# Performance work log

Hardware: AMD Instinct MI355X
Metric: run time of the kernel (lower is better)

The kernel has to match this reference:

```python
import jax, jax.numpy as jnp
import numpy as np

N = 8192       # nodes == in_channels (diff matrix is NxN)
DF = 256       # feature dim of z
E = 65536      # edges (unused by forward, kept for signature fidelity)
M = 4096       # len(reliable_negatives)
NEG = 10       # neg_samples
STEPS = 10     # num_diffusion_steps
TEMP = 0.2


def setup_inputs() -> dict:
    key = jax.random.key(0)
    k1, k2, k3, k4, k5 = jax.random.split(key, 5)
    z = jax.random.normal(k1, (N, DF), dtype=jnp.float32)
    # learned parameter; init positive-uniform so row sums are well conditioned
    diff_matrix = jax.random.uniform(k2, (N, N), dtype=jnp.float32)
    edge_index = jax.random.randint(k3, (2, E), 0, N)
    reliable_negatives = jax.random.randint(k4, (M,), 0, N)
    # deterministic stand-in for torch.randint(0, len(reliable_negatives), (neg_samples,))
    neg_idx = jax.random.randint(k5, (NEG,), 0, M)
    return {"z": z, "diff_matrix": diff_matrix, "edge_index": edge_index,
            "reliable_negatives": reliable_negatives, "neg_idx": neg_idx}


def _l2norm(x):
    # F.normalize(dim=1): divide by L2 norm clamped at 1e-12
    n = jnp.sqrt(jnp.sum(x * x, axis=1, keepdims=True))
    return x / jnp.maximum(n, 1e-12)


def reference(z, diff_matrix, edge_index, reliable_negatives, neg_idx):
    # 10-step loop: mm(inverse(diag(rowsum)), M) == row-wise reciprocal scaling
    dm = diff_matrix
    for _ in range(STEPS):
        dm = dm / jnp.sum(dm, axis=1, keepdims=True)  # [N, N]
    # (normalized_diff_matrix with +eps*I is computed in the original but unused)

    anchor = z                       # [N, DF]
    positive = dm @ z                # [N, DF] diffused features
    negative = z[neg_idx]            # [NEG, DF]

    a = _l2norm(anchor)
    p = _l2norm(positive)
    n = _l2norm(negative)

    pos_sim = jnp.sum(a * p, axis=1) / TEMP                 # [N]
    neg_sim = jnp.exp(jnp.einsum('nd,kd->nk', a, n) / TEMP)  # [N, NEG]
    loss = -jnp.log(jnp.exp(pos_sim) / (jnp.exp(pos_sim) + neg_sim.sum(axis=1))).mean()
    return loss
```

## Files before the change

### kernel.cpp

```cpp
#include <hip/hip_runtime.h>
#include <hip/hip_bf16.h>


typedef float f32x4 __attribute__((ext_vector_type(4)));
typedef short s16x8 __attribute__((ext_vector_type(8)));

#define NN 8192
#define DFF 256
#define NNEG 10

__device__ __forceinline__ unsigned short f2bf(float x) {
  return __builtin_bit_cast(unsigned short, __float2bfloat16(x));
}

__device__ __forceinline__ float bf2f(unsigned short u) {
  return __builtin_bit_cast(float, (unsigned int)u << 16);
}

__device__ __forceinline__ void gload_lds16(const void* g, void* l) {
  __builtin_amdgcn_global_load_lds(
      (const __attribute__((address_space(1))) void*)(void*)g,
      (__attribute__((address_space(3))) void*)l, 16, 0, 0);
}

__device__ __forceinline__ float dot4(float4 a, float4 b) {
  return a.x * b.x + a.y * b.y + a.z * b.z + a.w * b.w;
}

__global__ void k_pack(const float* __restrict__ z,
                       unsigned short* __restrict__ zp) {
  __shared__ float tile[64][65];
  const int bx = blockIdx.x;
  const int by = blockIdx.y;
  const int t = threadIdx.x;
  const int lc = t & 63, lq = t >> 6;
#pragma unroll
  for (int p = 0; p < 16; ++p) {
    const int kr = lq * 16 + p;
    tile[kr][lc] = z[(size_t)(bx * 64 + kr) * DFF + by * 64 + lc];
  }
  __syncthreads();
#pragma unroll
  for (int p2 = 0; p2 < 2; ++p2) {
    const int ko = lq * 2 + p2;
    s16x8 v;
#pragma unroll
    for (int ke = 0; ke < 8; ++ke) v[ke] = (short)f2bf(tile[ko * 8 + ke][lc]);
    const int chunk = bx * 2 + (ko >> 2);
    const int kw = ko & 3;
    const int d = by * 64 + lc;
    *(s16x8*)(zp + (size_t)chunk * 8192 + kw * 2048 + d * 8) = v;
  }
}

__global__ __launch_bounds__(512, 2) void k_gemm(const float* __restrict__ dm,
                                                 const unsigned short* __restrict__ zp,
                                                 unsigned short* __restrict__ part,
                                                 int KS) {
  __shared__ __align__(16) unsigned short sA[2][4096];
  __shared__ __align__(16) unsigned short sB[2][8192];
  const int bx = blockIdx.x;
  const int mtile = bx & 63;
  const int ks = bx >> 6;
  const int klen = NN / KS;
  const int k0 = ks * klen;
  const int c0 = k0 >> 5;
  const int steps = klen / 32;
  const int tid = threadIdx.x;
  const int w = tid >> 6;
  const int l = tid & 63;
  const int m0 = mtile * 128;

  const int arow = w * 16 + (l & 15);
  const int akw = l >> 4;
  const float* asrc = dm + (size_t)(m0 + arow) * NN + k0 + akw * 8;

  const int r16 = l & 15, kw = l >> 4;
  const int wm = w >> 2, wn = w & 3;

  f32x4 acc[4][4] = {};
  float4 a0, a1;

#define LOAD_A(t_)                                                             \
  {                                                                            \
    a0 = *(const float4*)(asrc + (t_)*32);                                     \
    a1 = *(const float4*)(asrc + (t_)*32 + 4);                                 \
  }

#define WRITE_A(s_)                                                           \
  {                                                                           \
    s16x8 h_;                                                                 \
    h_[0] = (short)f2bf(a0.x); h_[1] = (short)f2bf(a0.y);                     \
    h_[2] = (short)f2bf(a0.z); h_[3] = (short)f2bf(a0.w);                     \
    h_[4] = (short)f2bf(a1.x); h_[5] = (short)f2bf(a1.y);                     \
    h_[6] = (short)f2bf(a1.z); h_[7] = (short)f2bf(a1.w);                     \
    *(s16x8*)&sA[s_][akw * 1024 + arow * 8] = h_;                             \
  }

#define STAGE_B(t_, s_)                                                       \
  {                                                                           \
    const unsigned short* cs_ = zp + (size_t)(c0 + (t_)) * 8192;              \
    _Pragma("unroll") for (int q = 0; q < 2; ++q) {                           \
      const int piece_ = w * 2 + q;                      \
      gload_lds16((const char*)(cs_ + piece_ * 512) + l * 16,                 \
                  (char*)sB[s_] + piece_ * 1024);                             \
    }                                                                         \
  }

#define COMPUTE(s_)                                                           \
  {                                                                           \
    s16x8 af[4], bfr[4];                                                      \
    _Pragma("unroll") for (int mi = 0; mi < 4; ++mi) {                        \
      const int row_ = wm * 64 + mi * 16 + r16;                               \
      af[mi] = *(const s16x8*)&sA[s_][kw * 1024 + row_ * 8];                  \
    }                                                                         \
    _Pragma("unroll") for (int nj = 0; nj < 4; ++nj) {                        \
      const int col_ = wn * 64 + nj * 16 + r16;                               \
      bfr[nj] = *(const s16x8*)&sB[s_][kw * 2048 + col_ * 8];                 \
    }                                                                         \
    _Pragma("unroll") for (int mi = 0; mi < 4; ++mi)                          \
      _Pragma("unroll") for (int nj = 0; nj < 4; ++nj)                        \
        acc[mi][nj] = __builtin_amdgcn_mfma_f32_16x16x32_bf16(                \
            af[mi], bfr[nj], acc[mi][nj], 0, 0, 0);                           \
  }

  STAGE_B(0, 0);
  LOAD_A(0);
  WRITE_A(0);
  __syncthreads();

  for (int t = 0; t < steps; ++t) {
    const int cur = t & 1, nxt = cur ^ 1;
    if (t + 1 < steps) {
      LOAD_A(t + 1);
      STAGE_B(t + 1, nxt);
    }
    COMPUTE(cur);
    if (t + 1 < steps) WRITE_A(nxt);
    __syncthreads();
  }

#undef LOAD_A
#undef WRITE_A
#undef STAGE_B
#undef COMPUTE

  unsigned short* cb = part + (size_t)ks * NN * DFF;
#pragma unroll
  for (int mi = 0; mi < 4; ++mi)
#pragma unroll
    for (int nj = 0; nj < 4; ++nj) {
      const int col = wn * 64 + nj * 16 + r16;
      const int row0 = m0 + wm * 64 + mi * 16 + kw * 4;
#pragma unroll
      for (int r = 0; r < 4; ++r)
        cb[(size_t)(row0 + r) * DFF + col] = f2bf(acc[mi][nj][r]);
    }
}

__global__ __launch_bounds__(256) void k_loss(const float* __restrict__ z,
                                              const unsigned short* __restrict__ part,
                                              const int* __restrict__ neg_idx,
                                              float* __restrict__ lpart, int KS) {
  __shared__ float sneg[NNEG * DFF];
  __shared__ float swsum[4];
  const int t = threadIdx.x;
  const int w = t >> 6, l = t & 63;
  for (int k = w; k < NNEG; k += 4) {
    const int idx = neg_idx[k];
    float4 v = *(const float4*)(z + (size_t)idx * DFF + l * 4);
    float ss = dot4(v, v);
#pragma unroll
    for (int off = 32; off > 0; off >>= 1) ss += __shfl_xor(ss, off);
    const float s = 1.0f / fmaxf(sqrtf(ss), 1e-12f);
    float4 o;
    o.x = v.x * s; o.y = v.y * s; o.z = v.z * s; o.w = v.w * s;
    *(float4*)&sneg[k * DFF + l * 4] = o;
  }
  __syncthreads();
  const int gw = blockIdx.x * 4 + w;
  float lsum = 0.f;
  for (int rr = 0; rr < 8; ++rr) {
    const int i = gw * 8 + rr;
    const float4 a = *(const float4*)(z + (size_t)i * DFF + l * 4);
    float4 p; p.x = 0.f; p.y = 0.f; p.z = 0.f; p.w = 0.f;
    for (int ksp = 0; ksp < KS; ++ksp) {
      const ushort4 q =
          *(const ushort4*)(part + ((size_t)ksp * NN + i) * DFF + l * 4);
      p.x += bf2f(q.x); p.y += bf2f(q.y); p.z += bf2f(q.z); p.w += bf2f(q.w);
    }
    float vals[13];
    vals[0] = dot4(a, a);
    vals[1] = dot4(p, p);
    vals[2] = dot4(a, p);
#pragma unroll
    for (int k = 0; k < NNEG; ++k) {
      const float4 nv = *(const float4*)&sneg[k * DFF + l * 4];
      vals[3 + k] = dot4(a, nv);
    }
#pragma unroll
    for (int off = 32; off > 0; off >>= 1)
#pragma unroll
      for (int j = 0; j < 13; ++j) vals[j] += __shfl_xor(vals[j], off);
    const float na = fmaxf(sqrtf(vals[0]), 1e-12f);
    const float npp = fmaxf(sqrtf(vals[1]), 1e-12f);
    const float ps = vals[2] / (na * npp) * 5.0f;
    float S = 0.f;
#pragma unroll
    for (int k = 0; k < NNEG; ++k) S += expf(vals[3 + k] / na * 5.0f);
    lsum += logf(expf(ps) + S) - ps;
  }
  if (l == 0) swsum[w] = lsum;
  __syncthreads();
  if (t == 0) lpart[blockIdx.x] = swsum[0] + swsum[1] + swsum[2] + swsum[3];
}

__global__ void k_final(const float* __restrict__ lpart, float* __restrict__ out) {
  const int t = threadIdx.x;
  float v = lpart[t] + lpart[t + 64] + lpart[t + 128] + lpart[t + 192];
#pragma unroll
  for (int off = 32; off > 0; off >>= 1) v += __shfl_xor(v, off);
  if (t == 0) out[0] = v * (1.0f / (float)NN);
}

extern "C" void kernel_launch(void* const* d_in, const int* in_sizes, int n_in,
                              void* d_out, int out_size, void* d_ws, size_t ws_size,
                              hipStream_t stream) {
  const float* z = (const float*)d_in[0];
  const float* dm = (const float*)d_in[1];
  const int* neg_idx = (const int*)d_in[4];
  float* out = (float*)d_out;

  const size_t ZP = (size_t)NN * DFF * 2;
  auto need = [ZP](size_t ks) { return ZP + ks * (size_t)NN * DFF * 2 + 1024; };
  int KS = 8;
  if (ws_size < need(8)) KS = (ws_size >= need(4)) ? 4 : 2;

  char* ws = (char*)d_ws;
  unsigned short* zp = (unsigned short*)ws;
  unsigned short* part = (unsigned short*)(ws + ZP);
  float* lpart = (float*)(ws + ZP + (size_t)KS * NN * DFF * 2);

  k_pack<<<dim3(128, 4), 256, 0, stream>>>(z, zp);
  k_gemm<<<64 * KS, 512, 0, stream>>>(dm, zp, part, KS);
  k_loss<<<256, 256, 0, stream>>>(z, part, neg_idx, lpart, KS);
  k_final<<<1, 64, 0, stream>>>(lpart, out);
}
```

Baseline: 123.6 us.

## Switch LDS tiles to row-major k layout, reorder split-K blocks, nontemporal loads

Repacks z into a layout where each output column holds its 32 contiguous k values, and changes the A and B shared-memory tiles from k-group-major to row-major with 32 bf16 per row. The split-K index now varies fastest across block ids, so blocks that share an M tile run together. Loads of the fp32 diff matrix and stores of the bf16 partials use nontemporal hints to avoid polluting cache. The new LDS stride of 64 bytes per row may add bank conflicts on the 16-byte fragment reads.

```diff
diff --git a/kernel.cpp b/kernel.cpp
--- a/kernel.cpp
+++ b/kernel.cpp
@@ -40,17 +40,19 @@
     tile[kr][lc] = z[(size_t)(bx * 64 + kr) * DFF + by * 64 + lc];
   }
   __syncthreads();
-#pragma unroll
-  for (int p2 = 0; p2 < 2; ++p2) {
-    const int ko = lq * 2 + p2;
-    s16x8 v;
-#pragma unroll
-    for (int ke = 0; ke < 8; ++ke) v[ke] = (short)f2bf(tile[ko * 8 + ke][lc]);
-    const int chunk = bx * 2 + (ko >> 2);
-    const int kw = ko & 3;
-    const int d = by * 64 + lc;
-    *(s16x8*)(zp + (size_t)chunk * 8192 + kw * 2048 + d * 8) = v;
-  }
+  const int c2 = lq >> 1;
+  const int q = lq & 1;
+  s16x8 v0, v1;
+#pragma unroll
+  for (int ke = 0; ke < 8; ++ke)
+    v0[ke] = (short)f2bf(tile[c2 * 32 + q * 16 + ke][lc]);
+#pragma unroll
+  for (int ke = 0; ke < 8; ++ke)
+    v1[ke] = (short)f2bf(tile[c2 * 32 + q * 16 + 8 + ke][lc]);
+  unsigned short* dst =
+      zp + (size_t)(bx * 2 + c2) * 8192 + (by * 64 + lc) * 32 + q * 16;
+  *(s16x8*)dst = v0;
+  *(s16x8*)(dst + 8) = v1;
 }
 
 __global__ __launch_bounds__(512, 2) void k_gemm(const float* __restrict__ dm,
@@ -60,8 +62,8 @@
   __shared__ __align__(16) unsigned short sA[2][4096];
   __shared__ __align__(16) unsigned short sB[2][8192];
   const int bx = blockIdx.x;
-  const int mtile = bx & 63;
-  const int ks = bx >> 6;
+  const int ks = bx & (KS - 1);
+  const int mtile = bx / KS;
   const int klen = NN / KS;
   const int k0 = ks * klen;
   const int c0 = k0 >> 5;
@@ -79,49 +81,49 @@
   const int wm = w >> 2, wn = w & 3;
 
   f32x4 acc[4][4] = {};
-  float4 a0, a1;
-
-#define LOAD_A(t_)                                                             \
-  {                                                                            \
-    a0 = *(const float4*)(asrc + (t_)*32);                                     \
-    a1 = *(const float4*)(asrc + (t_)*32 + 4);                                 \
-  }
-
-#define WRITE_A(s_)                                                           \
+  f32x4 a0, a1;
+
+#define LOAD_A(t_)                                                            \
   {                                                                           \
-    s16x8 h_;                                                                 \
-    h_[0] = (short)f2bf(a0.x); h_[1] = (short)f2bf(a0.y);                     \
-    h_[2] = (short)f2bf(a0.z); h_[3] = (short)f2bf(a0.w);                     \
-    h_[4] = (short)f2bf(a1.x); h_[5] = (short)f2bf(a1.y);                     \
-    h_[6] = (short)f2bf(a1.z); h_[7] = (short)f2bf(a1.w);                     \
-    *(s16x8*)&sA[s_][akw * 1024 + arow * 8] = h_;                             \
-  }
-
-#define STAGE_B(t_, s_)                                                       \
-  {                                                                           \
-    const unsigned short* cs_ = zp + (size_t)(c0 + (t_)) * 8192;              \
-    _Pragma("unroll") for (int q = 0; q < 2; ++q) {                           \
-      const int piece_ = w * 2 + q;                      \
-      gload_lds16((const char*)(cs_ + piece_ * 512) + l * 16,                 \
-                  (char*)sB[s_] + piece_ * 1024);                             \
-    }                                                                         \
-  }
-
-#define COMPUTE(s_)                                                           \
-  {                                                                           \
-    s16x8 af[4], bfr[4];                                                      \
-    _Pragma("unroll") for (int mi = 0; mi < 4; ++mi) {                        \
-      const int row_ = wm * 64 + mi * 16 + r16;                               \
-      af[mi] = *(const s16x8*)&sA[s_][kw * 1024 + row_ * 8];                  \
-    }                                                                         \
-    _Pragma("unroll") for (int nj = 0; nj < 4; ++nj) {                        \
-      const int col_ = wn * 64 + nj * 16 + r16;                               \
-      bfr[nj] = *(const s16x8*)&sB[s_][kw * 2048 + col_ * 8];                 \
-    }                                                                         \
-    _Pragma("unroll") for (int mi = 0; mi < 4; ++mi)                          \
-      _Pragma("unroll") for (int nj = 0; nj < 4; ++nj)                        \
-        acc[mi][nj] = __builtin_amdgcn_mfma_f32_16x16x32_bf16(                \
-            af[mi], bfr[nj], acc[mi][nj], 0, 0, 0);                           \
+    a0 = __builtin_nontemporal_load((const f32x4*)(asrc + (t_)*32));          \
+    a1 = __builtin_nontemporal_load((const f32x4*)(asrc + (t_)*32 + 4));      \
+  }
+
+#define WRITE_A(s_)                                                          \
+  {                                                                          \
+    s16x8 h_;                                                                \
+    h_[0] = (short)f2bf(a0[0]); h_[1] = (short)f2bf(a0[1]);                  \
+    h_[2] = (short)f2bf(a0[2]); h_[3] = (short)f2bf(a0[3]);                  \
+    h_[4] = (short)f2bf(a1[0]); h_[5] = (short)f2bf(a1[1]);                  \
+    h_[6] = (short)f2bf(a1[2]); h_[7] = (short)f2bf(a1[3]);                  \
+    *(s16x8*)&sA[s_][arow * 32 + akw * 8] = h_;                              \
+  }
+
+#define STAGE_B(t_, s_)                                                      \
+  {                                                                          \
+    const unsigned short* cs_ = zp + (size_t)(c0 + (t_)) * 8192;             \
+    _Pragma("unroll") for (int q = 0; q < 2; ++q) {                          \
+      const int piece_ = w * 2 + q;                     \
+      gload_lds16((const char*)(cs_ + piece_ * 512) + l * 16,                \
+                  (char*)sB[s_] + piece_ * 1024);                            \
+    }                                                                        \
+  }
+
+#define COMPUTE(s_)                                                          \
+  {                                                                          \
+    s16x8 af[4], bfr[4];                                                     \
+    _Pragma("unroll") for (int mi = 0; mi < 4; ++mi) {                       \
+      const int row_ = wm * 64 + mi * 16 + r16;                              \
+      af[mi] = *(const s16x8*)&sA[s_][row_ * 32 + kw * 8];                   \
+    }                                                                        \
+    _Pragma("unroll") for (int nj = 0; nj < 4; ++nj) {                       \
+      const int col_ = wn * 64 + nj * 16 + r16;                              \
+      bfr[nj] = *(const s16x8*)&sB[s_][col_ * 32 + kw * 8];                  \
+    }                                                                        \
+    _Pragma("unroll") for (int mi = 0; mi < 4; ++mi)                         \
+      _Pragma("unroll") for (int nj = 0; nj < 4; ++nj)                       \
+        acc[mi][nj] = __builtin_amdgcn_mfma_f32_16x16x32_bf16(               \
+            af[mi], bfr[nj], acc[mi][nj], 0, 0, 0);                          \
   }
 
   STAGE_B(0, 0);
@@ -154,7 +156,8 @@
       const int row0 = m0 + wm * 64 + mi * 16 + kw * 4;
 #pragma unroll
       for (int r = 0; r < 4; ++r)
-        cb[(size_t)(row0 + r) * DFF + col] = f2bf(acc[mi][nj][r]);
+        __builtin_nontemporal_store(
+            f2bf(acc[mi][nj][r]), cb + (size_t)(row0 + r) * DFF + col);
     }
 }
 
```

After: 158.4 us. +28.1%, slower.
